# Optimization experiments

Hardware: AMD Instinct MI355X
Metric: run time of the kernel (lower is better)

The kernel has to match this reference:

```python
import jax, jax.numpy as jnp
import numpy as np

B, T, D = 2, 4096, 2048
HK, HV = 16, 32            # key heads, value heads (gqa_factor = 2)
AK, UV = 128, 128          # key head dim A, value head dim U
KEY_DIM = HK * AK          # 2048
VALUE_DIM = HV * UV        # 4096
CONV_DIM = 2 * KEY_DIM + VALUE_DIM  # 8192
KCONV = 4
CHUNK = 64
EPS = 1e-6


def setup_inputs() -> dict:
    key = jax.random.key(0)
    ks = jax.random.split(key, 10)
    s = lambda d: 1.0 / np.sqrt(d)
    return {
        "hidden": jax.random.normal(ks[0], (B, T, D), jnp.float32),
        "W_qkv": jax.random.normal(ks[1], (D, CONV_DIM), jnp.float32) * s(D),
        "W_z": jax.random.normal(ks[2], (D, VALUE_DIM), jnp.float32) * s(D),
        "W_b": jax.random.normal(ks[3], (D, HV), jnp.float32) * s(D),
        "W_a": jax.random.normal(ks[4], (D, HV), jnp.float32) * s(D),
        "conv_weight": jax.random.normal(ks[5], (CONV_DIM, KCONV), jnp.float32) * s(KCONV),
        "dt_bias": jnp.ones((HV,), jnp.float32),
        "A_log": jnp.log(jax.random.uniform(ks[6], (HV,), jnp.float32) * 16.0 + 1e-4),
        "norm_w": jnp.ones((UV,), jnp.float32),
        "W_out": jax.random.normal(ks[7], (VALUE_DIM, D), jnp.float32) * s(VALUE_DIM),
    }


def _l2norm(x, eps=1e-6):
    return x * jax.lax.rsqrt((x * x).sum(axis=-1, keepdims=True) + eps)


def _chunk_gated_delta_rule(q, k, v, g, beta, chunk_size=CHUNK):
    # inputs: q,k (B,T,Hv,A) l2-normalized below; v (B,T,Hv,U); g,beta (B,T,Hv)
    q = _l2norm(q)
    k = _l2norm(k)
    q, k, v = [x.transpose(0, 2, 1, 3).astype(jnp.float32) for x in (q, k, v)]
    beta = beta.transpose(0, 2, 1).astype(jnp.float32)
    g = g.transpose(0, 2, 1).astype(jnp.float32)
    Bs, H, Tt, A = k.shape
    U = v.shape[-1]
    pad = (chunk_size - Tt % chunk_size) % chunk_size
    if pad:
        q = jnp.pad(q, ((0, 0), (0, 0), (0, pad), (0, 0)))
        k = jnp.pad(k, ((0, 0), (0, 0), (0, pad), (0, 0)))
        v = jnp.pad(v, ((0, 0), (0, 0), (0, pad), (0, 0)))
        beta = jnp.pad(beta, ((0, 0), (0, 0), (0, pad)))
        g = jnp.pad(g, ((0, 0), (0, 0), (0, pad)))
    total = Tt + pad
    J = total // chunk_size
    q = q * (A ** -0.5)
    vb = v * beta[..., None]
    kb = k * beta[..., None]
    rs = lambda x, d: x.reshape(Bs, H, J, chunk_size, d)
    qj, kj, kbj = rs(q, A), rs(k, A), rs(kb, A)
    vbj = rs(vb, U)
    gj = jnp.cumsum(g.reshape(Bs, H, J, chunk_size), axis=-1)
    tril = jnp.tril(jnp.ones((chunk_size, chunk_size), jnp.float32))
    decay = jnp.exp((gj[..., :, None] - gj[..., None, :]) * tril) * tril
    upper = jnp.triu(jnp.ones((chunk_size, chunk_size), bool))
    attn = -(jnp.einsum('BHJLA,BHJMA->BHJLM', kbj, kj) * decay)
    attn = jnp.where(upper, 0.0, attn)

    def correction_step(i, a):  # sequential UT transform over rows
        row = a[..., i, :]
        return a.at[..., i, :].set(row + jnp.einsum('...j,...jk->...k', row, a))

    attn = jax.lax.fori_loop(1, chunk_size, correction_step, attn)
    attn = attn + jnp.eye(chunk_size, dtype=jnp.float32)
    v_corr = jnp.einsum('BHJLM,BHJMU->BHJLU', attn, vbj)
    k_cd = jnp.einsum('BHJLM,BHJMA->BHJLA', attn, kbj * jnp.exp(gj)[..., None])
    upper1 = jnp.triu(jnp.ones((chunk_size, chunk_size), bool), k=1)

    def chunk_step(st, j):  # st: (B,H,A,U) recurrent state
        qc, kc = qj[:, :, j], kj[:, :, j]
        vc, gc, kcd = v_corr[:, :, j], gj[:, :, j], k_cd[:, :, j]
        dm = decay[:, :, j]
        intra = jnp.einsum('BHLA,BHMA->BHLM', qc, kc) * dm
        intra = jnp.where(upper1, 0.0, intra)
        v_new = vc - jnp.einsum('BHLA,BHAU->BHLU', kcd, st)
        inter = jnp.exp(gc)[..., None] * jnp.einsum('BHLA,BHAU->BHLU', qc, st)
        out_c = inter + jnp.einsum('BHLM,BHMU->BHLU', intra, v_new)
        k_dec = kc * jnp.exp(gc[:, :, -1:] - gc)[..., None]
        st = st * jnp.exp(gc[:, :, -1])[..., None, None] + jnp.einsum('BHMA,BHMU->BHAU', k_dec, v_new)
        return st, out_c

    st0 = jnp.zeros((Bs, H, A, U), jnp.float32)
    _, outs = jax.lax.scan(chunk_step, st0, jnp.arange(J))
    out = outs.transpose(1, 2, 0, 3, 4).reshape(Bs, H, total, U)[:, :, :Tt]
    return out.transpose(0, 2, 1, 3)  # (B,T,H,U)


def _forward(hidden, W_qkv, W_z, W_b, W_a, conv_weight, dt_bias, A_log, norm_w, W_out):
    Bs, Tl, _ = hidden.shape
    mixed = (hidden @ W_qkv).transpose(0, 2, 1)  # (B, C, T)
    z = hidden @ W_z                              # (B, T, value_dim)
    b = hidden @ W_b                              # (B, T, Hv)
    a = hidden @ W_a                              # (B, T, Hv)
    # causal depthwise conv1d (kernel KCONV) + SiLU
    xp = jnp.pad(mixed, ((0, 0), (0, 0), (KCONV - 1, 0)))
    conv = sum(conv_weight[None, :, kk:kk + 1] * xp[:, :, kk:kk + Tl] for kk in range(KCONV))
    mixed = jax.nn.silu(conv).transpose(0, 2, 1)  # (B, T, C)
    q, k, v = jnp.split(mixed, [KEY_DIM, 2 * KEY_DIM], axis=-1)
    q = q.reshape(Bs, Tl, HK, AK)
    k = k.reshape(Bs, Tl, HK, AK)
    v = v.reshape(Bs, Tl, HV, UV)
    beta = jax.nn.sigmoid(b)
    g = -jnp.exp(A_log.astype(jnp.float32)) * jax.nn.softplus(a.astype(jnp.float32) + dt_bias)
    gqa = HV // HK
    q = jnp.repeat(q, gqa, axis=2)  # matches broadcast_to+reshape interleaving
    k = jnp.repeat(k, gqa, axis=2)
    core = _chunk_gated_delta_rule(q, k, v, g, beta)  # (B,T,Hv,U)
    # gated RMSNorm per value head (Mamba2/Qwen3-Next style: gate then norm)
    x = core.reshape(-1, UV)
    zf = z.reshape(-1, UV).astype(jnp.float32)
    xg = x * jax.nn.silu(zf)
    normed = norm_w * (xg * jax.lax.rsqrt((xg * xg).mean(-1, keepdims=True) + EPS))
    return normed.reshape(Bs, Tl, VALUE_DIM).astype(hidden.dtype) @ W_out


def reference(hidden, W_qkv, W_z, W_b, W_a, conv_weight, dt_bias, A_log, norm_w, W_out):
    return _forward(hidden, W_qkv, W_z, W_b, W_a, conv_weight, dt_bias, A_log, norm_w, W_out)
```

## Files before the change

kernel.cpp:

```cpp
#include <hip/hip_runtime.h>

#define B_   2
#define T_   4096
#define D_   2048
#define HV_  32
#define AK_  128
#define UV_  128
#define KD_  2048
#define VD_  4096
#define CD_  8192
#define CHK  64
#define NCH  (T_/CHK)

typedef __attribute__((ext_vector_type(4))) float  f32x4;
typedef __attribute__((ext_vector_type(8))) short  short8;
typedef __attribute__((ext_vector_type(4))) short  short4b;
typedef __attribute__((ext_vector_type(8))) unsigned short u16x8;
typedef __attribute__((ext_vector_type(4))) unsigned short u16x4;

__device__ __forceinline__ float bf2f(unsigned short u) {
  return __uint_as_float(((unsigned)u) << 16);
}
__device__ __forceinline__ unsigned short f2bf(float f) {
  unsigned u = __float_as_uint(f);
  return (unsigned short)((u + 0x7fffu + ((u >> 16) & 1u)) >> 16);
}
__device__ __forceinline__ void gload16(const void* g, void* l) {
  __builtin_amdgcn_global_load_lds((const __attribute__((address_space(1))) void*)g,
                                   (__attribute__((address_space(3))) void*)l, 16, 0, 0);
}

__global__ __launch_bounds__(256) void k_transpose(const float* __restrict__ src,
                                                   unsigned short* __restrict__ dst,
                                                   int K, int N) {
  __shared__ float tile[32][33];
  int k0 = blockIdx.x * 32, n0 = blockIdx.y * 32;
  int tx = threadIdx.x, ty = threadIdx.y;
  #pragma unroll
  for (int i = 0; i < 32; i += 8)
    tile[ty + i][tx] = src[(size_t)(k0 + ty + i) * N + n0 + tx];
  __syncthreads();
  #pragma unroll
  for (int i = 0; i < 32; i += 8)
    dst[(size_t)(n0 + ty + i) * K + k0 + tx] = f2bf(tile[tx][ty + i]);
}

__device__ __forceinline__ void storeC(float* p, float v) { *p = v; }
__device__ __forceinline__ void storeC(unsigned short* p, float v) { *p = f2bf(v); }

template <bool AGL, typename CT>
__global__ __launch_bounds__(256, 2) void k_gemm(const void* __restrict__ Av,
                                                 const unsigned short* __restrict__ BT,
                                                 CT* __restrict__ C, int N, int K) {
  __shared__ __attribute__((aligned(16))) short As[128 * 64];
  __shared__ __attribute__((aligned(16))) short Bs[256 * 64];
  const int tid  = threadIdx.x;
  const int bid  = blockIdx.x;
  const int tb   = bid & 63;
  const size_t bm = (size_t)(8 * (tb & 7) + (tb >> 3)) * 128;
  const size_t bn = (size_t)(bid >> 6) * 256;
  const int lane = tid & 63;
  const int wave = tid >> 6;
  const int wm = (wave >> 1) * 64;
  const int wn = (wave & 1) * 64;
  const int fr = lane & 15;
  const int kg = lane >> 4;
  const int lr = lane >> 3, lc8 = (lane & 7) * 8;
  const short* gb = (const short*)BT + (bn + wave * 64 + lr) * (size_t)K + lc8;
  short* lB = &Bs[wave * 64 * 64];
  const short* gab = (const short*)Av + (bm + wave * 32 + lr) * (size_t)K + lc8;
  short* lA = &As[wave * 32 * 64];

  f32x4 acc[4][8];
  #pragma unroll
  for (int i = 0; i < 4; ++i)
    #pragma unroll
    for (int j2 = 0; j2 < 8; ++j2) acc[i][j2] = (f32x4){0.f, 0.f, 0.f, 0.f};

  for (int kt = 0; kt < K; kt += 64) {
    __syncthreads();
    #pragma unroll
    for (int p = 0; p < 8; ++p)
      gload16(gb + kt + (size_t)(8 * p) * K, lB + (8 * p) * 64);
    if constexpr (AGL) {
      #pragma unroll
      for (int p = 0; p < 4; ++p)
        gload16(gab + kt + (size_t)(8 * p) * K, lA + (8 * p) * 64);
    } else {
      const float* Ag = (const float*)Av + bm * (size_t)K;
      #pragma unroll
      for (int s = 0; s < 8; ++s) {
        int ch = s * 256 + tid;
        int r = ch >> 4, c4 = (ch & 15) * 4;
        float4 v = *(const float4*)(Ag + (size_t)r * K + kt + c4);
        short4b sv = { (short)f2bf(v.x), (short)f2bf(v.y), (short)f2bf(v.z), (short)f2bf(v.w) };
        *(short4b*)&As[r * 64 + c4] = sv;
      }
    }
    __syncthreads();
    #pragma unroll
    for (int kk = 0; kk < 2; ++kk) {
      short8 af[4], bfr[8];
      #pragma unroll
      for (int mi = 0; mi < 4; ++mi) af[mi] = *(const short8*)&As[(wm + mi*16 + fr)*64 + kk*32 + kg*8];
      #pragma unroll
      for (int ni = 0; ni < 4; ++ni) {
        bfr[ni]     = *(const short8*)&Bs[(wn + ni*16 + fr)*64 + kk*32 + kg*8];
        bfr[4 + ni] = *(const short8*)&Bs[(128 + wn + ni*16 + fr)*64 + kk*32 + kg*8];
      }
      #pragma unroll
      for (int mi = 0; mi < 4; ++mi)
        #pragma unroll
        for (int ni = 0; ni < 8; ++ni)
          acc[mi][ni] = __builtin_amdgcn_mfma_f32_16x16x32_bf16(af[mi], bfr[ni], acc[mi][ni], 0, 0, 0);
    }
  }
  #pragma unroll
  for (int mi = 0; mi < 4; ++mi)
    #pragma unroll
    for (int ni = 0; ni < 8; ++ni) {
      size_t row = bm + wm + mi * 16 + kg * 4;
      size_t col = bn + (ni >= 4 ? 128 : 0) + wn + (ni & 3) * 16 + fr;
      #pragma unroll
      for (int e = 0; e < 4; ++e) storeC(&C[(row + e) * (size_t)N + col], acc[mi][ni][e]);
    }
}

__global__ __launch_bounds__(256) void k_beta_g(const float* __restrict__ hidden,
                                                const float* __restrict__ Wb,
                                                const float* __restrict__ Wa,
                                                const float* __restrict__ dt_bias,
                                                const float* __restrict__ A_log,
                                                float* __restrict__ betab,
                                                float* __restrict__ gbuf,
                                                unsigned short* __restrict__ hidb) {
  const int tid = threadIdx.x;
  const int r = tid >> 5, hh = tid & 31;
  const size_t bt = (size_t)blockIdx.x * 8 + r;
  const float* hrow = hidden + bt * D_;
  float sb = 0.f, sa = 0.f;
  for (int d = 0; d < D_; ++d) {
    float hv = hrow[d];
    sb += hv * Wb[d * 32 + hh];
    sa += hv * Wa[d * 32 + hh];
  }
  unsigned short* hb = hidb + bt * D_ + hh * 64;
  #pragma unroll
  for (int d2 = 0; d2 < 64; d2 += 8) {
    float4 v0 = *(const float4*)(hrow + hh * 64 + d2);
    float4 v1 = *(const float4*)(hrow + hh * 64 + d2 + 4);
    u16x8 o = { f2bf(v0.x), f2bf(v0.y), f2bf(v0.z), f2bf(v0.w),
                f2bf(v1.x), f2bf(v1.y), f2bf(v1.z), f2bf(v1.w) };
    *(u16x8*)(hb + d2) = o;
  }
  float beta = 1.f / (1.f + __expf(-sb));
  float xg = sa + dt_bias[hh];
  float sp = (xg > 20.f) ? xg : log1pf(__expf(xg));
  float g = -__expf(A_log[hh]) * sp;
  int b = (int)(bt >> 12);
  int t = (int)(bt & (T_ - 1));
  size_t o = ((size_t)b * HV_ + hh) * T_ + t;
  betab[o] = beta;
  gbuf[o] = g;
}

__global__ __launch_bounds__(256) void k_qkv(const unsigned short* __restrict__ mqk,
                                             const float* __restrict__ cw,
                                             unsigned short* __restrict__ qn,
                                             unsigned short* __restrict__ kn) {
  const int row = blockIdx.x;
  const int b = row >> 12, t = row & (T_ - 1);
  const int tid = threadIdx.x;
  const int c0 = tid * 16;
  float4 w[16];
  #pragma unroll
  for (int e = 0; e < 16; ++e) w[e] = *(const float4*)&cw[(size_t)(c0 + e) * 4];
  float acc[16];
  #pragma unroll
  for (int e = 0; e < 16; ++e) acc[e] = 0.f;
  #pragma unroll
  for (int p = 0; p < 4; ++p) {
    int ts = t - 3 + p;
    if (ts < 0) continue;
    const unsigned short* src = mqk + (size_t)(b * T_ + ts) * 4096 + c0;
    u16x8 v0 = *(const u16x8*)src;
    u16x8 v1 = *(const u16x8*)(src + 8);
    #pragma unroll
    for (int e = 0; e < 8; ++e) {
      acc[e]     += bf2f(v0[e]) * ((const float*)&w[e])[p];
      acc[8 + e] += bf2f(v1[e]) * ((const float*)&w[8 + e])[p];
    }
  }
  float s = 0.f;
  #pragma unroll
  for (int e = 0; e < 16; ++e) {
    float x = acc[e];
    x = x / (1.f + __expf(-x));
    acc[e] = x;
    s += x * x;
  }
  s += __shfl_xor(s, 1); s += __shfl_xor(s, 2); s += __shfl_xor(s, 4);
  float sc = rsqrtf(s + 1e-6f);
  bool isq = (c0 < KD_);
  if (isq) sc *= 0.08838834764831845f;
  int ch = isq ? c0 : (c0 - KD_);
  int hk = ch >> 7, cc = ch & 127;
  unsigned short* dst = (isq ? qn : kn) + ((size_t)(b * 16 + hk) * T_ + t) * 128 + cc;
  u16x8 o0, o1;
  #pragma unroll
  for (int e = 0; e < 8; ++e) { o0[e] = f2bf(acc[e] * sc); o1[e] = f2bf(acc[8 + e] * sc); }
  *(u16x8*)dst = o0;
  *(u16x8*)(dst + 8) = o1;
}

__global__ __launch_bounds__(256) void k_prep(const unsigned short* __restrict__ kn,
                                              const float* __restrict__ gbuf,
                                              const float* __restrict__ betab,
                                              unsigned short* __restrict__ Tg,
                                              unsigned short* __restrict__ knT,
                                              float* __restrict__ gjc) {
  __shared__ __attribute__((aligned(16))) unsigned short kl[CHK][136];
  __shared__ float L[CHK][65];
  __shared__ float W1[CHK][65];
  __shared__ float gj[CHK], bet[CHK];
  const int tid = threadIdx.x;
  const int blk = blockIdx.x;
  const int j = blk & 63, h = (blk >> 6) & 31, b = blk >> 11;
  const int hk = h >> 1;
  const int t0 = j * CHK;
  const int lane = tid & 63, wv = tid >> 6;
  const int fr = lane & 15, kg = lane >> 4;
  const int ty = tid >> 4, tx = tid & 15;

  const unsigned short* ksrc = kn + ((size_t)(b * 16 + hk) * T_ + t0) * 128;
  #pragma unroll
  for (int p = 0; p < 4; ++p) {
    int id = p * 256 + tid;
    int r = id >> 4, c = (id & 15) * 8;
    *(u16x8*)&kl[r][c] = *(const u16x8*)(ksrc + (size_t)r * 128 + c);
  }
  if (tid < 64) {
    float gval = gbuf[((size_t)b * HV_ + h) * T_ + t0 + tid];
    #pragma unroll
    for (int off = 1; off < 64; off <<= 1) {
      float o = __shfl_up(gval, off);
      if (tid >= off) gval += o;
    }
    gj[tid] = gval;
    gjc[((size_t)(b * HV_ + h) * NCH + j) * 64 + tid] = gval;
    bet[tid] = betab[((size_t)b * HV_ + h) * T_ + t0 + tid];
  }
  __syncthreads();

  if ((h & 1) == 0) {
    unsigned short* kd = knT + ((size_t)(b * 16 + hk) * NCH + j) * 8192;
    int a = tid >> 1, l0 = (tid & 1) * 32;
    u16x8 o[4];
    #pragma unroll
    for (int i = 0; i < 32; ++i) ((unsigned short*)o)[i] = kl[l0 + i][a];
    #pragma unroll
    for (int p = 0; p < 4; ++p) *(u16x8*)(kd + a * 64 + l0 + p * 8) = o[p];
  }

  {
    const int s0 = 16 * wv;
    f32x4 ag[4];
    #pragma unroll
    for (int mt = 0; mt < 4; ++mt) ag[mt] = (f32x4){0.f, 0.f, 0.f, 0.f};
    #pragma unroll
    for (int ks = 0; ks < 4; ++ks) {
      short8 af = *(const short8*)&kl[s0 + fr][ks * 32 + kg * 8];
      #pragma unroll
      for (int mt = 0; mt < 4; ++mt) {
        short8 bfv = *(const short8*)&kl[mt * 16 + fr][ks * 32 + kg * 8];
        ag[mt] = __builtin_amdgcn_mfma_f32_16x16x32_bf16(af, bfv, ag[mt], 0, 0, 0);
      }
    }
    #pragma unroll
    for (int mt = 0; mt < 4; ++mt)
      #pragma unroll
      for (int e = 0; e < 4; ++e) {
        int l = s0 + kg * 4 + e, m = mt * 16 + fr;
        L[l][m] = (l > m) ? (-bet[l] * ag[mt][e] * __expf(gj[l] - gj[m])) : 0.f;
      }
  }
  __syncthreads();
  for (int i = tid; i < CHK * CHK; i += 256) { int l = i >> 6, m = i & 63; W1[l][m] = L[l][m]; }
  __syncthreads();

  #pragma unroll
  for (int dk = 1; dk <= 5; ++dk) {
    const int p2 = 1 << (dk - 1);
    float s4[4][4];
    #pragma unroll
    for (int i = 0; i < 4; ++i)
      #pragma unroll
      for (int c = 0; c < 4; ++c) s4[i][c] = 0.f;
    {
      const int hi = 16 * wv + 15 - p2;
      for (int jm = p2; jm <= hi; ++jm) {
        float wl[4], wr[4];
        #pragma unroll
        for (int i = 0; i < 4; ++i) wl[i] = W1[ty * 4 + i][jm];
        #pragma unroll
        for (int c = 0; c < 4; ++c) wr[c] = W1[jm][tx * 4 + c];
        #pragma unroll
        for (int i = 0; i < 4; ++i)
          #pragma unroll
          for (int c = 0; c < 4; ++c) s4[i][c] += wl[i] * wr[c];
      }
    }
    __syncthreads();
    #pragma unroll
    for (int i = 0; i < 4; ++i)
      #pragma unroll
      for (int c = 0; c < 4; ++c) W1[ty * 4 + i][tx * 4 + c] = s4[i][c];
    __syncthreads();
    float pu[4][4];
    #pragma unroll
    for (int i = 0; i < 4; ++i)
      #pragma unroll
      for (int c = 0; c < 4; ++c) pu[i][c] = L[ty * 4 + i][tx * 4 + c] + W1[ty * 4 + i][tx * 4 + c];
    {
      const int hi = 16 * wv + 14;
      for (int jm = p2 * 2; jm <= hi; ++jm) {
        float pl[4], wr[4];
        #pragma unroll
        for (int i = 0; i < 4; ++i) pl[i] = L[ty * 4 + i][jm];
        #pragma unroll
        for (int c = 0; c < 4; ++c) wr[c] = W1[jm][tx * 4 + c];
        #pragma unroll
        for (int i = 0; i < 4; ++i)
          #pragma unroll
          for (int c = 0; c < 4; ++c) pu[i][c] += pl[i] * wr[c];
      }
    }
    __syncthreads();
    #pragma unroll
    for (int i = 0; i < 4; ++i)
      #pragma unroll
      for (int c = 0; c < 4; ++c) L[ty * 4 + i][tx * 4 + c] = pu[i][c];
    __syncthreads();
  }
  unsigned short* td = Tg + (size_t)blk * 4096;
  #pragma unroll
  for (int pp = 0; pp < 2; ++pp) {
    int id = pp * 256 + tid;
    int l = id >> 3, m8 = (id & 7) * 8;
    u16x8 o;
    #pragma unroll
    for (int e = 0; e < 8; ++e) {
      float v = L[l][m8 + e] + ((l == m8 + e) ? 1.f : 0.f);
      o[e] = f2bf(v);
    }
    *(u16x8*)(td + (size_t)l * 64 + m8) = o;
  }
}

__global__ __launch_bounds__(256) void k_scan(const unsigned short* __restrict__ qn,
                                              const unsigned short* __restrict__ kn,
                                              const unsigned short* __restrict__ mv,
                                              const unsigned short* __restrict__ Tg,
                                              const unsigned short* __restrict__ knT,
                                              const float* __restrict__ gjc,
                                              const float* __restrict__ betab,
                                              const float* __restrict__ cw,
                                              unsigned short* __restrict__ xout) {
  __shared__ __attribute__((aligned(16))) unsigned short kl[CHK][136];
  __shared__ __attribute__((aligned(16))) unsigned short intr[CHK][72];
  __shared__ float ST[16][132];
  __shared__ __attribute__((aligned(16))) unsigned short SbT[16][136];
  __shared__ __attribute__((aligned(16))) unsigned short vbT[16][72], vnT[16][72], vndT[16][72];
  __shared__ float gj[CHK], bet[CHK], eg[CHK], edec[CHK], beg[CHK];

  const int tid = threadIdx.x;
  const int blk = blockIdx.x;
  const int xcd  = blk & 7;
  const int slot = blk >> 3;
  const int g    = xcd + 8 * (slot >> 4);
  const int wgrp = slot & 15;
  const int b  = g >> 4;
  const int hk = g & 15;
  const int h  = hk * 2 + (wgrp >> 3);
  const int us = wgrp & 7;
  const int u0 = us * 16;
  const int lane = tid & 63, wv = tid >> 6;
  const int fr = lane & 15, kg = lane >> 4;
  const int s0 = 16 * wv;

  const int cvl = tid >> 2, c4 = (tid & 3) * 4;
  float4 wv4[4];
  #pragma unroll
  for (int i = 0; i < 4; ++i)
    wv4[i] = *(const float4*)&cw[(size_t)(2 * KD_ + h * 128 + u0 + c4 + i) * 4];

  for (int i = tid; i < 16 * 132; i += 256) (&ST[0][0])[i] = 0.f;

  const unsigned short* qsrc = qn + (size_t)(b * 16 + hk) * T_ * 128;
  const unsigned short* ksrc = kn + (size_t)(b * 16 + hk) * T_ * 128;
  const unsigned short* tsrc = Tg + (size_t)((b * 32 + h) * 64) * 4096;
  const unsigned short* knsrc = knT + (size_t)(b * 16 + hk) * NCH * 8192;
  const float* gsrc = gjc + (size_t)(b * 32 + h) * 4096;
  const float* bsrc = betab + ((size_t)b * HV_ + h) * T_;

  const int rr = tid >> 4, cc8 = (tid & 15) * 8;

  u16x8 krg[4];
  u16x4 vld[4];
  float g_r = 0.f, b_r = 0.f;

  #pragma unroll
  for (int p = 0; p < 4; ++p) {
    int r = p * 16 + rr;
    krg[p] = *(const u16x8*)(ksrc + (size_t)r * 128 + cc8);
  }
  if (tid < 64) { g_r = gsrc[tid]; b_r = bsrc[tid]; }
  #pragma unroll
  for (int p = 0; p < 4; ++p) {
    int ts = cvl - 3 + p;
    vld[p] = (ts >= 0) ? *(const u16x4*)(mv + (size_t)(b * T_ + ts) * 4096 + h * 128 + u0 + c4)
                       : (u16x4){0, 0, 0, 0};
  }
  #pragma unroll
  for (int p = 0; p < 4; ++p) {
    int r = p * 16 + rr;
    *(u16x8*)&kl[r][cc8] = krg[p];
  }
  if (tid < 64) { gj[tid] = g_r; bet[tid] = b_r; }
  __syncthreads();

  for (int j = 0; j < NCH; ++j) {
    const int t0 = j * CHK;
    short8 kr[2][2], qf[4], tf[2];
    #pragma unroll
    for (int t2 = 0; t2 < 2; ++t2) {
      int a0 = wv * 32 + t2 * 16;
      #pragma unroll
      for (int ks = 0; ks < 2; ++ks)
        kr[t2][ks] = *(const short8*)(knsrc + (size_t)j * 8192 + (a0 + fr) * 64 + ks * 32 + kg * 8);
    }
    #pragma unroll
    for (int ks = 0; ks < 4; ++ks)
      qf[ks] = *(const short8*)(qsrc + (size_t)(t0 + s0 + fr) * 128 + ks * 32 + kg * 8);
    #pragma unroll
    for (int ks = 0; ks < 2; ++ks)
      tf[ks] = *(const short8*)(tsrc + (size_t)j * 4096 + (s0 + fr) * 64 + ks * 32 + kg * 8);
    if (j + 1 < NCH) {
      const int t1 = t0 + CHK;
      #pragma unroll
      for (int p = 0; p < 4; ++p) {
        int r = p * 16 + rr;
        krg[p] = *(const u16x8*)(ksrc + (size_t)(t1 + r) * 128 + cc8);
      }
      if (tid < 64) { g_r = gsrc[(j + 1) * 64 + tid]; b_r = bsrc[t1 + tid]; }
    }
    if (tid < 64) {
      float gl = gj[63];
      float e = __expf(gj[tid]);
      eg[tid] = e;
      edec[tid] = __expf(gl - gj[tid]);
      beg[tid] = bet[tid] * e;
    }
    {
      float a4[4] = {0.f, 0.f, 0.f, 0.f};
      #pragma unroll
      for (int p = 0; p < 4; ++p)
        #pragma unroll
        for (int i = 0; i < 4; ++i) a4[i] += bf2f(vld[p][i]) * ((const float*)&wv4[i])[p];
      float be = bet[cvl];
      #pragma unroll
      for (int i = 0; i < 4; ++i) {
        float x = a4[i];
        x = x / (1.f + __expf(-x)) * be;
        vbT[c4 + i][cvl] = f2bf(x);
      }
    }
    if (j + 1 < NCH) {
      #pragma unroll
      for (int p = 0; p < 4; ++p) {
        int ts = t0 + CHK + cvl - 3 + p;
        vld[p] = *(const u16x4*)(mv + (size_t)(b * T_ + ts) * 4096 + h * 128 + u0 + c4);
      }
    }
    {
      int u = tid >> 4, a8 = (tid & 15) * 8;
      u16x8 o;
      #pragma unroll
      for (int e = 0; e < 8; ++e) o[e] = f2bf(ST[u][a8 + e]);
      *(u16x8*)&SbT[u][a8] = o;
    }
    __syncthreads();

    {
      f32x4 ag[4];
      #pragma unroll
      for (int mt = 0; mt < 4; ++mt) ag[mt] = (f32x4){0.f, 0.f, 0.f, 0.f};
      #pragma unroll
      for (int ks = 0; ks < 4; ++ks) {
        #pragma unroll
        for (int mt = 0; mt < 4; ++mt) {
          short8 bfv = *(const short8*)&kl[mt * 16 + fr][ks * 32 + kg * 8];
          ag[mt] = __builtin_amdgcn_mfma_f32_16x16x32_bf16(qf[ks], bfv, ag[mt], 0, 0, 0);
        }
      }
      #pragma unroll
      for (int mt = 0; mt < 4; ++mt)
        #pragma unroll
        for (int e = 0; e < 4; ++e) {
          int l = s0 + kg * 4 + e, m = mt * 16 + fr;
          float v = (l >= m) ? (ag[mt][e] * __expf(gj[l] - gj[m])) : 0.f;
          intr[l][m] = f2bf(v);
        }
    }
    {
      f32x4 a1 = (f32x4){0.f, 0.f, 0.f, 0.f};
      #pragma unroll
      for (int ks = 0; ks < 4; ++ks) {
        short8 af = *(const short8*)&kl[s0 + fr][ks * 32 + kg * 8];
        short8 bfv = *(const short8*)&SbT[fr][ks * 32 + kg * 8];
        a1 = __builtin_amdgcn_mfma_f32_16x16x32_bf16(af, bfv, a1, 0, 0, 0);
      }
      #pragma unroll
      for (int e = 0; e < 4; ++e) {
        int l = s0 + kg * 4 + e;
        float vm = bf2f(vbT[fr][l]) - beg[l] * a1[e];
        vbT[fr][l] = f2bf(vm);
      }
    }
    __syncthreads();
    {
      f32x4 a2 = (f32x4){0.f, 0.f, 0.f, 0.f};
      #pragma unroll
      for (int ks = 0; ks < 2; ++ks) {
        short8 bfv = *(const short8*)&vbT[fr][ks * 32 + kg * 8];
        a2 = __builtin_amdgcn_mfma_f32_16x16x32_bf16(tf[ks], bfv, a2, 0, 0, 0);
      }
      #pragma unroll
      for (int e = 0; e < 4; ++e) {
        int l = s0 + kg * 4 + e;
        vnT[fr][l]  = f2bf(a2[e]);
        vndT[fr][l] = f2bf(a2[e] * edec[l]);
      }
    }
    __syncthreads();
    {
      f32x4 ai = (f32x4){0.f, 0.f, 0.f, 0.f};
      f32x4 aq = (f32x4){0.f, 0.f, 0.f, 0.f};
      #pragma unroll
      for (int ks = 0; ks < 2; ++ks) {
        short8 af = *(const short8*)&intr[s0 + fr][ks * 32 + kg * 8];
        short8 bfv = *(const short8*)&vnT[fr][ks * 32 + kg * 8];
        ai = __builtin_amdgcn_mfma_f32_16x16x32_bf16(af, bfv, ai, 0, 0, 0);
      }
      #pragma unroll
      for (int ks = 0; ks < 4; ++ks) {
        short8 bfv = *(const short8*)&SbT[fr][ks * 32 + kg * 8];
        aq = __builtin_amdgcn_mfma_f32_16x16x32_bf16(qf[ks], bfv, aq, 0, 0, 0);
      }
      #pragma unroll
      for (int e = 0; e < 4; ++e) {
        int l = s0 + kg * 4 + e;
        float o = eg[l] * aq[e] + ai[e];
        xout[((size_t)(b * T_ + t0 + l) * HV_ + h) * UV_ + u0 + fr] = f2bf(o);
      }
    }
    {
      float egl = eg[63];
      #pragma unroll
      for (int t2 = 0; t2 < 2; ++t2) {
        int a0 = wv * 32 + t2 * 16;
        f32x4 cf;
        #pragma unroll
        for (int e = 0; e < 4; ++e) cf[e] = ST[kg * 4 + e][a0 + fr] * egl;
        #pragma unroll
        for (int ks = 0; ks < 2; ++ks) {
          short8 af = *(const short8*)&vndT[fr][ks * 32 + kg * 8];
          cf = __builtin_amdgcn_mfma_f32_16x16x32_bf16(af, kr[t2][ks], cf, 0, 0, 0);
        }
        #pragma unroll
        for (int e = 0; e < 4; ++e) ST[kg * 4 + e][a0 + fr] = cf[e];
      }
    }
    __syncthreads();
    if (j + 1 < NCH) {
      #pragma unroll
      for (int p = 0; p < 4; ++p) {
        int r = p * 16 + rr;
        *(u16x8*)&kl[r][cc8] = krg[p];
      }
      if (tid < 64) { gj[tid] = g_r; bet[tid] = b_r; }
    }
    __syncthreads();
  }
}

__global__ __launch_bounds__(256) void k_gate_norm(const unsigned short* __restrict__ x,
                                                   const unsigned short* __restrict__ z,
                                                   const float* __restrict__ nw,
                                                   unsigned short* __restrict__ out) {
  const int row = blockIdx.x * 4 + (threadIdx.x >> 6);
  const int lane = threadIdx.x & 63;
  const unsigned short* xp = x + (size_t)row * UV_;
  const unsigned short* zp = z + (size_t)row * UV_;
  float x0 = bf2f(xp[lane]), x1 = bf2f(xp[lane + 64]);
  float z0 = bf2f(zp[lane]), z1 = bf2f(zp[lane + 64]);
  float g0 = x0 * (z0 / (1.f + __expf(-z0)));
  float g1 = x1 * (z1 / (1.f + __expf(-z1)));
  float s = g0 * g0 + g1 * g1;
  #pragma unroll
  for (int off = 32; off > 0; off >>= 1) s += __shfl_xor(s, off);
  float r = rsqrtf(s * (1.f / UV_) + 1e-6f);
  out[(size_t)row * UV_ + lane]      = f2bf(nw[lane] * g0 * r);
  out[(size_t)row * UV_ + lane + 64] = f2bf(nw[lane + 64] * g1 * r);
}

extern "C" void kernel_launch(void* const* d_in, const int* in_sizes, int n_in,
                              void* d_out, int out_size, void* d_ws, size_t ws_size,
                              hipStream_t stream) {
  (void)in_sizes; (void)n_in; (void)out_size; (void)ws_size;
  const float* hidden  = (const float*)d_in[0];
  const float* W_qkv   = (const float*)d_in[1];
  const float* W_z     = (const float*)d_in[2];
  const float* W_b     = (const float*)d_in[3];
  const float* W_a     = (const float*)d_in[4];
  const float* conv_w  = (const float*)d_in[5];
  const float* dt_bias = (const float*)d_in[6];
  const float* A_log   = (const float*)d_in[7];
  const float* norm_w  = (const float*)d_in[8];
  const float* W_out   = (const float*)d_in[9];
  float* out = (float*)d_out;

  const size_t MB = 1048576ull;
  char* w = (char*)d_ws;
  unsigned short* wqkvT = (unsigned short*)(w);
  unsigned short* Tg    = (unsigned short*)(w);
  unsigned short* mqk   = (unsigned short*)(w + 32 * MB);
  unsigned short* xcore = (unsigned short*)(w + 32 * MB);
  unsigned short* mv    = (unsigned short*)(w + 96 * MB);
  unsigned short* normed= (unsigned short*)(w + 96 * MB);
  unsigned short* hidb  = (unsigned short*)(w + 160 * MB);
  unsigned short* qn    = (unsigned short*)(w + 160 * MB);
  unsigned short* zb    = (unsigned short*)(w + 160 * MB);
  unsigned short* knT   = (unsigned short*)(w + 192 * MB);
  unsigned short* kn    = (unsigned short*)(w + 224 * MB);
  unsigned short* wzT   = (unsigned short*)(w + 224 * MB);
  unsigned short* woutT = (unsigned short*)(w + 240 * MB);
  float*          betab = (float*)(w + 288 * MB);
  float*          gbuf  = (float*)(w + 289 * MB);
  float*          gjc   = (float*)(w + 290 * MB);

  k_beta_g<<<dim3(B_ * T_ / 8), 256, 0, stream>>>(hidden, W_b, W_a, dt_bias, A_log, betab, gbuf, hidb);
  k_transpose<<<dim3(D_ / 32, CD_ / 32), dim3(32, 8), 0, stream>>>(W_qkv, wqkvT, D_, CD_);
  k_gemm<true, unsigned short><<<dim3(64 * 16), 256, 0, stream>>>(hidb, wqkvT, mqk, 4096, 2048);
  k_gemm<true, unsigned short><<<dim3(64 * 16), 256, 0, stream>>>(hidb, wqkvT + (size_t)4096 * 2048, mv, 4096, 2048);
  k_qkv<<<dim3(B_ * T_), 256, 0, stream>>>(mqk, conv_w, qn, kn);
  k_prep<<<dim3(B_ * HV_ * NCH), 256, 0, stream>>>(kn, gbuf, betab, Tg, knT, gjc);
  k_scan<<<dim3(B_ * HV_ * 8), 256, 0, stream>>>(qn, kn, mv, Tg, knT, gjc, betab, conv_w, xcore);
  k_transpose<<<dim3(D_ / 32, VD_ / 32), dim3(32, 8), 0, stream>>>(W_z, wzT, D_, VD_);
  k_gemm<false, unsigned short><<<dim3(64 * 16), 256, 0, stream>>>(hidden, wzT, zb, 4096, 2048);
  k_transpose<<<dim3(VD_ / 32, D_ / 32), dim3(32, 8), 0, stream>>>(W_out, woutT, VD_, D_);
  k_gate_norm<<<dim3(B_ * T_ * HV_ / 4), 256, 0, stream>>>(xcore, zb, norm_w, normed);
  k_gemm<true, float><<<dim3(64 * 8), 256, 0, stream>>>(normed, woutT, out, 2048, 4096);
}
```

Measured before the change: 1.602 ms.

## Add triple-buffered async-load GEMM and use it for bf16-input projections

```diff
diff --git a/kernel.cpp b/kernel.cpp
--- a/kernel.cpp
+++ b/kernel.cpp
@@ -47,6 +47,94 @@
 
 __device__ __forceinline__ void storeC(float* p, float v) { *p = v; }
 __device__ __forceinline__ void storeC(unsigned short* p, float v) { *p = f2bf(v); }
+
+template <typename CT>
+__global__ __launch_bounds__(256, 2) void k_gemmp(const unsigned short* __restrict__ A,
+                                                  const unsigned short* __restrict__ BT,
+                                                  CT* __restrict__ C, int N, int K) {
+  __shared__ __attribute__((aligned(16))) short As[3][128 * 32];
+  __shared__ __attribute__((aligned(16))) short Bs[3][256 * 32];
+  const int tid  = threadIdx.x;
+  const int bid  = blockIdx.x;
+  const int tb   = bid & 63;
+  const size_t bm = (size_t)(8 * (tb & 7) + (tb >> 3)) * 128;
+  const size_t bn = (size_t)(bid >> 6) * 256;
+  const int lane = tid & 63;
+  const int wave = tid >> 6;
+  const int wm = (wave >> 1) * 64;
+  const int wn = (wave & 1) * 64;
+  const int fr = lane & 15;
+  const int kg = lane >> 4;
+  const int lr = lane >> 2, lc8 = (lane & 3) * 8;
+  const short* gA = (const short*)A  + (bm + wave * 32 + lr) * (size_t)K + lc8;
+  const short* gB = (const short*)BT + (bn + wave * 64 + lr) * (size_t)K + lc8;
+  const int lbA = (wave * 32) * 32;
+  const int lbB = (wave * 64) * 32;
+
+  f32x4 acc[4][8];
+  #pragma unroll
+  for (int i = 0; i < 4; ++i)
+    #pragma unroll
+    for (int j2 = 0; j2 < 8; ++j2) acc[i][j2] = (f32x4){0.f, 0.f, 0.f, 0.f};
+
+  const int nt = K >> 5;
+  #pragma unroll
+  for (int t = 0; t < 2; ++t) {
+    const int kt = t * 32;
+    #pragma unroll
+    for (int p = 0; p < 2; ++p)
+      gload16(gA + kt + (size_t)(16 * p) * K, &As[t][lbA + p * 16 * 32]);
+    #pragma unroll
+    for (int p = 0; p < 4; ++p)
+      gload16(gB + kt + (size_t)(16 * p) * K, &Bs[t][lbB + p * 16 * 32]);
+  }
+
+  int cur = 0;
+  for (int i = 0; i < nt; ++i) {
+    if (i + 1 < nt) { asm volatile("s_waitcnt vmcnt(6)" ::: "memory"); }
+    else            { asm volatile("s_waitcnt vmcnt(0)" ::: "memory"); }
+    __builtin_amdgcn_sched_barrier(0);
+    __builtin_amdgcn_s_barrier();
+    __builtin_amdgcn_sched_barrier(0);
+    if (i + 2 < nt) {
+      const int nb = (cur + 2 >= 3) ? cur - 1 : cur + 2;
+      const int kt = (i + 2) * 32;
+      #pragma unroll
+      for (int p = 0; p < 2; ++p)
+        gload16(gA + kt + (size_t)(16 * p) * K, &As[nb][lbA + p * 16 * 32]);
+      #pragma unroll
+      for (int p = 0; p < 4; ++p)
+        gload16(gB + kt + (size_t)(16 * p) * K, &Bs[nb][lbB + p * 16 * 32]);
+    }
+    {
+      short8 af[4], bfr[8];
+      #pragma unroll
+      for (int mi = 0; mi < 4; ++mi) af[mi] = *(const short8*)&As[cur][(wm + mi*16 + fr)*32 + kg*8];
+      #pragma unroll
+      for (int ni = 0; ni < 4; ++ni) {
+        bfr[ni]     = *(const short8*)&Bs[cur][(wn + ni*16 + fr)*32 + kg*8];
+        bfr[4 + ni] = *(const short8*)&Bs[cur][(128 + wn + ni*16 + fr)*32 + kg*8];
+      }
+      __builtin_amdgcn_s_setprio(1);
+      #pragma unroll
+      for (int mi = 0; mi < 4; ++mi)
+        #pragma unroll
+        for (int ni = 0; ni < 8; ++ni)
+          acc[mi][ni] = __builtin_amdgcn_mfma_f32_16x16x32_bf16(af[mi], bfr[ni], acc[mi][ni], 0, 0, 0);
+      __builtin_amdgcn_s_setprio(0);
+    }
+    cur = (cur == 2) ? 0 : cur + 1;
+  }
+  #pragma unroll
+  for (int mi = 0; mi < 4; ++mi)
+    #pragma unroll
+    for (int ni = 0; ni < 8; ++ni) {
+      size_t row = bm + wm + mi * 16 + kg * 4;
+      size_t col = bn + (ni >= 4 ? 128 : 0) + wn + (ni & 3) * 16 + fr;
+      #pragma unroll
+      for (int e = 0; e < 4; ++e) storeC(&C[(row + e) * (size_t)N + col], acc[mi][ni][e]);
+    }
+}
 
 template <bool AGL, typename CT>
 __global__ __launch_bounds__(256, 2) void k_gemm(const void* __restrict__ Av,
@@ -651,8 +739,8 @@
 
   k_beta_g<<<dim3(B_ * T_ / 8), 256, 0, stream>>>(hidden, W_b, W_a, dt_bias, A_log, betab, gbuf, hidb);
   k_transpose<<<dim3(D_ / 32, CD_ / 32), dim3(32, 8), 0, stream>>>(W_qkv, wqkvT, D_, CD_);
-  k_gemm<true, unsigned short><<<dim3(64 * 16), 256, 0, stream>>>(hidb, wqkvT, mqk, 4096, 2048);
-  k_gemm<true, unsigned short><<<dim3(64 * 16), 256, 0, stream>>>(hidb, wqkvT + (size_t)4096 * 2048, mv, 4096, 2048);
+  k_gemmp<unsigned short><<<dim3(64 * 16), 256, 0, stream>>>(hidb, wqkvT, mqk, 4096, 2048);
+  k_gemmp<unsigned short><<<dim3(64 * 16), 256, 0, stream>>>(hidb, wqkvT + (size_t)4096 * 2048, mv, 4096, 2048);
   k_qkv<<<dim3(B_ * T_), 256, 0, stream>>>(mqk, conv_w, qn, kn);
   k_prep<<<dim3(B_ * HV_ * NCH), 256, 0, stream>>>(kn, gbuf, betab, Tg, knT, gjc);
   k_scan<<<dim3(B_ * HV_ * 8), 256, 0, stream>>>(qn, kn, mv, Tg, knT, gjc, betab, conv_w, xcore);
@@ -660,5 +748,5 @@
   k_gemm<false, unsigned short><<<dim3(64 * 16), 256, 0, stream>>>(hidden, wzT, zb, 4096, 2048);
   k_transpose<<<dim3(VD_ / 32, D_ / 32), dim3(32, 8), 0, stream>>>(W_out, woutT, VD_, D_);
   k_gate_norm<<<dim3(B_ * T_ * HV_ / 4), 256, 0, stream>>>(xcore, zb, norm_w, normed);
-  k_gemm<true, float><<<dim3(64 * 8), 256, 0, stream>>>(normed, woutT, out, 2048, 4096);
-}
+  k_gemmp<float><<<dim3(64 * 8), 256, 0, stream>>>(normed, woutT, out, 2048, 4096);
+}
```

Result: no change. 1.615 ms (+0.8%).
